# Kernel tuning notes

Measured on AMD Instinct MI355X. Metric: run time of the kernel, lower is better.

The kernel has to match this reference:

```python
import jax, jax.numpy as jnp
import numpy as np

N_LIG, N_PROT, K = 1024, 8192, 48
N = N_LIG + N_PROT
HID, FEAT, DEPTH = 256, 32, 5
NF = 6                      # sinusoid frequencies -> 12-dim distance embedding
EDGE_DIM = 4 * NF           # per-block dist emb (12) + top-level dist emb (12)
NORM = 5.0                  # agg_norm_factor
_FREQS = (2.0 * np.pi * 4.0 ** np.arange(NF) / 15.0).astype(np.float32)

def sin_emb(d2):
    # d2: [E,1] squared distances -> [E, 2*NF] sinusoidal embedding
    d = jnp.sqrt(d2 + 1e-8)
    x = d * _FREQS
    return jnp.concatenate([jnp.sin(x), jnp.cos(x)], axis=-1)

def knn_edges(coors):
    # KNN (k=48, no self loops) restricted to ligand query nodes (first N_LIG),
    # matching edges[:, :N_lig*k] slicing of knn_graph(flow='target_to_source').
    c = jax.lax.stop_gradient(coors)
    lig = c[:N_LIG]
    d2 = jnp.sum((lig[:, None, :] - c[None, :, :]) ** 2, axis=-1)  # [N_LIG, N]
    d2 = d2.at[jnp.arange(N_LIG), jnp.arange(N_LIG)].set(jnp.inf)
    _, idx = jax.lax.top_k(-d2, K)                                  # [N_LIG, K]
    row = jnp.repeat(jnp.arange(N_LIG), K)
    col = idx.reshape(-1)
    return row, col

def egnn(h, x, row, col, W_in, b_in, W_out, b_out, edge_W1, edge_b1, edge_W2, edge_b2, att_W, att_b, node_W1, node_b1, node_W2, node_b2, coord_W1, coord_b1, coord_W2, coord_b2, coord_W3):
    # EDM-style EGNN: per block 1 GCL (edge MLP + attention gate + node MLP residual)
    # followed by an equivariant coordinate update; sin distance embedding.
    emb0 = sin_emb(jnp.sum((x[row] - x[col]) ** 2, axis=-1, keepdims=True))
    h = h @ W_in + b_in
    for l in range(DEPTH):
        diff = x[row] - x[col]                         # [E,3]
        d2 = jnp.sum(diff ** 2, axis=-1, keepdims=True)
        cdiff = diff / (jnp.sqrt(d2 + 1e-8) + 1.0)     # norm_constant = 1
        ea = jnp.concatenate([sin_emb(d2), emb0], axis=-1)  # [E, EDGE_DIM]
        m = jax.nn.silu(jnp.concatenate([h[row], h[col], ea], axis=-1) @ edge_W1[l] + edge_b1[l])
        m = jax.nn.silu(m @ edge_W2[l] + edge_b2[l])
        m = m * jax.nn.sigmoid(m @ att_W[l] + att_b[l])         # attention gate
        agg = jax.ops.segment_sum(m, row, num_segments=N) / NORM
        u = jax.nn.silu(jnp.concatenate([h, agg], axis=-1) @ node_W1[l] + node_b1[l])
        h = h + (u @ node_W2[l] + node_b2[l])                    # residual node update
        c = jax.nn.silu(jnp.concatenate([h[row], h[col], ea], axis=-1) @ coord_W1[l] + coord_b1[l])  # use_latest_h
        c = jax.nn.silu(c @ coord_W2[l] + coord_b2[l])
        x = x + jax.ops.segment_sum(cdiff * (c @ coord_W3[l]), row, num_segments=N) / NORM
    return h @ W_out + b_out, x

def setup_inputs():
    key = jax.random.key(0)
    ks = jax.random.split(key, 24)
    f32 = jnp.float32
    def nrm(i, shape, scale=0.05):
        return jax.random.normal(ks[i], shape, dtype=f32) * scale
    return {
        'protein_positions': nrm(0, (N_PROT, 3), 3.0),
        'protein_ele': jax.random.randint(ks[1], (N_PROT,), 0, 5),
        'protein_amino_acid': jax.random.randint(ks[2], (N_PROT,), 0, 20),
        'protein_is_backbone': jax.random.randint(ks[3], (N_PROT,), 0, 2),
        'Xt_pos': nrm(4, (N_LIG, 3), 1.0),
        'Xt_features': nrm(5, (N_LIG, FEAT), 1.0),
        't': jax.random.randint(ks[6], (N_LIG,), 0, 1000),
        'Wt_time': nrm(7, (1000, 8), 1.0),
        'W_ele': nrm(8, (5, 16), 1.0),
        'W_aa': nrm(9, (20, 16), 1.0),
        'W_bb': nrm(10, (2, 8), 1.0),
        'W_in': nrm(11, (40, HID)), 'b_in': jnp.zeros((HID,), f32),
        'W_out': nrm(12, (HID, FEAT)), 'b_out': jnp.zeros((FEAT,), f32),
        'edge_W1': nrm(13, (DEPTH, 2 * HID + EDGE_DIM, HID)), 'edge_b1': jnp.zeros((DEPTH, HID), f32),
        'edge_W2': nrm(14, (DEPTH, HID, HID)), 'edge_b2': jnp.zeros((DEPTH, HID), f32),
        'att_W': nrm(15, (DEPTH, HID, 1)), 'att_b': jnp.zeros((DEPTH, 1), f32),
        'node_W1': nrm(16, (DEPTH, 2 * HID, HID)), 'node_b1': jnp.zeros((DEPTH, HID), f32),
        'node_W2': nrm(17, (DEPTH, HID, HID)), 'node_b2': jnp.zeros((DEPTH, HID), f32),
        'coord_W1': nrm(18, (DEPTH, 2 * HID + EDGE_DIM, HID)), 'coord_b1': jnp.zeros((DEPTH, HID), f32),
        'coord_W2': nrm(19, (DEPTH, HID, HID)), 'coord_b2': jnp.zeros((DEPTH, HID), f32),
        'coord_W3': nrm(20, (DEPTH, HID, 1), 0.001),
        'pos_w': jnp.ones((1, 1), f32),
    }

def reference(protein_positions, protein_ele, protein_amino_acid, protein_is_backbone, Xt_pos, Xt_features, t, Wt_time, W_ele, W_aa, W_bb, W_in, b_in, W_out, b_out, edge_W1, edge_b1, edge_W2, edge_b2, att_W, att_b, node_W1, node_b1, node_W2, node_b2, coord_W1, coord_b1, coord_W2, coord_b2, coord_W3, pos_w):
    prot_feat = jnp.concatenate([W_ele[protein_ele], W_aa[protein_amino_acid], W_bb[protein_is_backbone]], axis=-1)  # [N_PROT,40]
    feats = jnp.concatenate([jnp.concatenate([Xt_features, Wt_time[t]], axis=-1), prot_feat], axis=0)  # [N,40]
    coors = jnp.concatenate([Xt_pos, protein_positions], axis=0)  # [N,3]
    row, col = knn_edges(coors)
    h, x = egnn(feats, coors, row, col, W_in, b_in, W_out, b_out, edge_W1, edge_b1, edge_W2, edge_b2, att_W, att_b, node_W1, node_b1, node_W2, node_b2, coord_W1, coord_b1, coord_W2, coord_b2, coord_W3)
    # pos_linear: Linear(1,1,bias=False) applied elementwise == scalar multiply
    return x[:N_LIG] * pos_w[0, 0], h[:N_LIG]
```

## Files before the change

kernel.cpp:

```cpp
#include <hip/hip_runtime.h>
#include <hip/hip_bf16.h>
#include <math.h>

#define N_LIGC 1024
#define NTOT 9216
#define KNN 48
#define HID 256
#define DEPTHC 5
#define ETOT (N_LIGC*KNN)
#define KBINS 4096

typedef unsigned short u16;
typedef __attribute__((ext_vector_type(8))) short bf16x8;
typedef __attribute__((ext_vector_type(4))) float f32x4;

__device__ __forceinline__ float freq_f(int i){
  double p = (double)(1 << (2*i));
  return (float)((2.0*3.14159265358979323846)*p/15.0);
}
__device__ __forceinline__ float silu_f(float v){
  return v*__builtin_amdgcn_rcpf(1.0f+__expf(-v));
}
__device__ __forceinline__ float sigm_f(float v){
  return __builtin_amdgcn_rcpf(1.0f+__expf(-v));
}
// ... 19 lines not shown
  int Kt = Kp >> 5;
  int k0 = rest2 % Kt;
  int layer = rest2 / Kt;
  int kq = lane >> 4, nl = lane & 15;
  int kb = k0*32 + kq*8, n = n0*16 + nl;
  u16 o[8];
  #pragma unroll
  for (int j=0;j<8;j++){
    int k = kb + j;
    float v = (k < Keff) ? src[((size_t)layer*srcK + kOff + k)*N + n] : 0.f;
    o[j] = f2b_p(v);
  }
  *(uint4*)(dst + (size_t)idx*8) = *(uint4*)o;
}

__global__ __launch_bounds__(256) void k_packall(
    const float* eW1, const float* eW2, const float* nW1, const float* nW2,
    const float* cW1, const float* cW2, const float* Wout,
    u16* eW1abP, u16* eW1cP, u16* eW2p, u16* nW1p, u16* nW2p,
    u16* cW1abP, u16* cW1cP, u16* cW2p, u16* WoutP)
{
  int idx = blockIdx.x*256 + threadIdx.x;
  if (idx < 81920){ pack_one(eW1, eW1abP, 536, 0,   512, 512, 256, idx); return; } idx -= 81920;
  if (idx < 5120 ){ pack_one(eW1, eW1cP,  536, 512, 24,  32,  256, idx); return; } idx -= 5120;
  if (idx < 40960){ pack_one(eW2, eW2p,   256, 0,   256, 256, 256, idx); return; } idx -= 40960;
  if (idx < 81920){ pack_one(nW1, nW1p,   512, 0,   512, 512, 256, idx); return; } idx -= 81920;
  if (idx < 40960){ pack_one(nW2, nW2p,   256, 0,   256, 256, 256, idx); return; } idx -= 40960;
  if (idx < 81920){ pack_one(cW1, cW1abP, 536, 0,   512, 512, 256, idx); return; } idx -= 81920;
  if (idx < 5120 ){ pack_one(cW1, cW1cP,  536, 512, 24,  32,  256, idx); return; } idx -= 5120;
  if (idx < 40960){ pack_one(cW2, cW2p,   256, 0,   256, 256, 256, idx); return; } idx -= 40960;
  if (idx < 1024 ){ pack_one(Wout, WoutP, 256, 0,   256, 256, 32,  idx); return; }
}

__global__ __launch_bounds__(256) void k_embed_hinit(
    const float* __restrict__ protPos, const int* __restrict__ protEle,
    const int* __restrict__ protAA, const int* __restrict__ protBB,
    const float* __restrict__ XtPos, const float* __restrict__ XtFeat,
    const int* __restrict__ tArr, const float* __restrict__ WtTime,
    const float* __restrict__ Wele, const float* __restrict__ Waa,
    const float* __restrict__ Wbb,
    const float* __restrict__ Win, const float* __restrict__ bin,
    float* __restrict__ X0, float* __restrict__ X1,
    float* __restrict__ h, u16* __restrict__ h_bf)
{
  __shared__ float sF[8*40];
  int blk=blockIdx.x, tid=threadIdx.x;
  int n0=blk*8;
  for (int x=tid; x<344; x+=256){
    if (x < 320){
      int n = x/40, k = x%40;
      int node = n0+n;
      float v;
      if (node < N_LIGC){
        if (k < 32) v = XtFeat[node*32+k];
        else        v = WtTime[tArr[node]*8 + (k-32)];
      } else {
        int p = node - N_LIGC;
        if (k < 16)      v = Wele[protEle[p]*16 + k];
        else if (k < 32) v = Waa[protAA[p]*16 + (k-16)];
        else             v = Wbb[protBB[p]*8 + (k-32)];
      }
// ... 11 lines not shown
  #pragma unroll
  for (int n=0;n<8;n++) acc[n]=b;
  for (int k=0;k<40;k++){
    float w=Win[k*HID+tid];
    #pragma unroll
    for (int n=0;n<8;n++) acc[n]+=sF[n*40+k]*w;
  }
  #pragma unroll
  for (int n=0;n<8;n++){
    h[(size_t)(n0+n)*HID+tid]=acc[n];
    h_bf[(size_t)(n0+n)*HID+tid]=f2b_p(acc[n]);
  }
}

__global__ __launch_bounds__(256) void k_knn(const float* __restrict__ X,
    int* __restrict__ col, float* __restrict__ emb0)
{
  __shared__ unsigned int hist[KBINS];
  __shared__ unsigned int part[256];
  __shared__ float selD[KNN];
  __shared__ int   candI[512];
  __shared__ float candV[512];
  __shared__ int sB, sCless, sNeed, sNsel, sNcand;
  int b = blockIdx.x, tid = threadIdx.x;
  for (int i=tid;i<KBINS;i+=256) hist[i]=0u;
  if (tid==0){ sNsel=0; sNcand=0; }
  float px = X[b*3+0], py = X[b*3+1], pz = X[b*3+2];
  __syncthreads();
  #pragma unroll 4
  for (int j=0;j<36;j++){
    int i = tid + 256*j;
// ... 71 lines not shown
        int   os = __shfl_down(bslot, off);
        if (ov < bv || (ov==bv && oi<bi)){ bv=ov; bi=oi; bslot=os; }
      }
      int wslot = __shfl(bslot, 0);
      if (tid==0){ col[b*KNN+base+it]=bi; selD[base+it]=bv; }
      if ((wslot & 63) == tid) cv[wslot >> 6] = INFINITY;
    }
  }
  __syncthreads();
  if (tid < KNN){
    float d = sqrtf(selD[tid] + 1e-8f);
    int base = (b*KNN+tid)*12;
    #pragma unroll
    for (int i=0;i<6;i++){
      float fr = freq_f(i);
      emb0[base+i]   = sinf(d*fr);
      emb0[base+6+i] = cosf(d*fr);
    }
  }
}

__global__ __launch_bounds__(256) void k_pq(const u16* __restrict__ h_bf,
    const u16* __restrict__ Wab, float* __restrict__ R, u16* __restrict__ Qb, int l)
{
  __shared__ __align__(16) u16 sA[32*264];
  int blk=blockIdx.x, tid=threadIdx.x;
  int lane=tid&63, ng=tid>>6, quad=lane>>4, nl=lane&15;
  for (int t=tid; t<32*32; t+=256){
    int i=t>>5, q=t&31;
    uint4 v = ((const uint4*)(h_bf + (size_t)(blk*32+i)*HID))[q];
    *(uint4*)(sA + i*264 + q*8) = v;
  }
// ... 59 lines not shown
    #pragma unroll
    for (int nt=0;nt<4;nt++){
      int n = ng*64 + nt*16 + nl;
      #pragma unroll
      for (int r=0;r<4;r++){
        int node = blk*32 + mt*16 + quad*4 + r;
        R[(size_t)node*HID + n] = aR[mt][nt][r];
      }
    }
  }
}

__global__ __launch_bounds__(256,4) void k_comb_edge(
    const u16* __restrict__ Qb, const float* __restrict__ R,
    const float* __restrict__ xc,
    const int* __restrict__ colIdx, const float* __restrict__ emb0,
    const u16* __restrict__ W1cP, const float* __restrict__ B1,
    const u16* __restrict__ W2p, const float* __restrict__ B2,
    const float* __restrict__ attW, const float* __restrict__ attB,
    u16* __restrict__ agg_bf, int l)
{
  __shared__ __align__(16) u16 sQ[48*264];
  __shared__ __align__(16) u16 sEA[48*40];
  __shared__ float sR[256];
  __shared__ int sCol[48];
  __shared__ float sD[48];
  __shared__ float sSig[48];
  __shared__ float sDot[48][4];

  int row = blockIdx.x, tid = threadIdx.x;
  int lane = tid & 63, ng = tid >> 6;
// ... 2 lines not shown
  if (tid < 48) sCol[tid] = colIdx[(size_t)row*KNN + tid];
  sR[tid] = R[(size_t)row*HID + tid];
  __syncthreads();
  for (int t = tid; t < 48*32; t += 256){
    int e = t >> 5, q = t & 31;
    uint4 v = ((const uint4*)(Qb + (size_t)sCol[e]*HID))[q];
    *(uint4*)(sQ + e*264 + q*8) = v;
  }
  if (tid < 48){
    int cg = sCol[tid];
    float dx = xc[row*3+0]-xc[cg*3+0];
    float dy = xc[row*3+1]-xc[cg*3+1];
    float dz = xc[row*3+2]-xc[cg*3+2];
    float d = sqrtf(dx*dx+dy*dy+dz*dz + 1e-8f);
    sD[tid] = d;
    u16* ea = sEA + tid*40;
    #pragma unroll
    for (int i=0;i<12;i++) ea[12+i] = f2b_p(emb0[((size_t)row*KNN + tid)*12 + i]);
    #pragma unroll
    for (int i=24;i<32;i++) ea[i] = 0;
  }
  __syncthreads();
  for (int t=tid; t<288; t+=256){
    int e = t/6, i = t - 6*e;
    float fr = 0.41887903f * (float)(1 << (2*i));
    float x = sD[e]*fr;
    u16* ea = sEA + e*40;
    ea[i]   = f2b(__sinf(x));
    ea[6+i] = f2b(__cosf(x));
  }
  __syncthreads();

  f32x4 zero4 = {0.f,0.f,0.f,0.f};
// ... 113 lines not shown
    sgv[mt][r] = sSig[mt*16 + quad*4 + r];
  #pragma unroll
  for (int nt=0;nt<4;nt++){
    float a = 0.f;
    #pragma unroll
    for (int mt=0;mt<3;mt++)
    #pragma unroll
    for (int r=0;r<4;r++)
      a += acc2[mt][nt][r]*sgv[mt][r];
    a += __shfl_xor(a, 16);
    a += __shfl_xor(a, 32);
    if (quad == 0) agg_bf[(size_t)row*HID + ng*64 + nt*16 + nl] = f2b(a*0.2f);
  }
}

__global__ __launch_bounds__(256) void k_node(
    float* __restrict__ h, u16* __restrict__ h_bf,
    const u16* __restrict__ agg_bf,
    const u16* __restrict__ W1p, const float* __restrict__ B1,
    const u16* __restrict__ W2p, const float* __restrict__ B2,
    const u16* __restrict__ cWab, u16* __restrict__ QbC, float* __restrict__ RC,
    const u16* __restrict__ eWabN, u16* __restrict__ QbE, float* __restrict__ RE, int doE,
    const u16* __restrict__ WoutP, const float* __restrict__ bout,
    float* __restrict__ outH, int doOut, int l)
{
  __shared__ __align__(16) u16 sA[32*520];
  __shared__ __align__(16) u16 sU[32*264];
  u16* sH = sA;
  int blk=blockIdx.x, tid=threadIdx.x;
  int lane=tid&63, wv=tid>>6, quad=lane>>4, nl=lane&15;
  for (int t=tid; t<32*64; t+=256){
    int i=t>>6, q=t&63;
    int node = blk*32+i;
    uint4 v;
    if (q<32) v = ((const uint4*)(h_bf + (size_t)node*HID))[q];
    else if (node < N_LIGC) v = ((const uint4*)(agg_bf + (size_t)node*HID))[q-32];
    else { v.x=0u; v.y=0u; v.z=0u; v.w=0u; }
    *(uint4*)(sA + i*520 + q*8) = v;
  }
  __syncthreads();
  f32x4 zero4 = {0.f,0.f,0.f,0.f};
  f32x4 acc[2][4];
  #pragma unroll
  for (int i=0;i<2;i++){ acc[i][0]=zero4; acc[i][1]=zero4; acc[i][2]=zero4; acc[i][3]=zero4; }
  const u16* Wp = W1p + (size_t)l*512*HID;
  #pragma unroll 2
  for (int k0=0;k0<16;k0++){
    bf16x8 a0 = *(const bf16x8*)(sA + (0*16+nl)*520 + k0*32 + quad*8);
    bf16x8 a1 = *(const bf16x8*)(sA + (1*16+nl)*520 + k0*32 + quad*8);
    const u16* wb = Wp + ((size_t)(k0*16 + wv*4)*64 + lane)*8;
    bf16x8 b0 = *(const bf16x8*)(wb);
    bf16x8 b1 = *(const bf16x8*)(wb + 512);
    bf16x8 b2 = *(const bf16x8*)(wb + 1024);
    bf16x8 b3 = *(const bf16x8*)(wb + 1536);
    acc[0][0]=__builtin_amdgcn_mfma_f32_16x16x32_bf16(a0,b0,acc[0][0],0,0,0);
    acc[0][1]=__builtin_amdgcn_mfma_f32_16x16x32_bf16(a0,b1,acc[0][1],0,0,0);
    acc[0][2]=__builtin_amdgcn_mfma_f32_16x16x32_bf16(a0,b2,acc[0][2],0,0,0);
    acc[0][3]=__builtin_amdgcn_mfma_f32_16x16x32_bf16(a0,b3,acc[0][3],0,0,0);
    acc[1][0]=__builtin_amdgcn_mfma_f32_16x16x32_bf16(a1,b0,acc[1][0],0,0,0);
    acc[1][1]=__builtin_amdgcn_mfma_f32_16x16x32_bf16(a1,b1,acc[1][1],0,0,0);
    acc[1][2]=__builtin_amdgcn_mfma_f32_16x16x32_bf16(a1,b2,acc[1][2],0,0,0);
    acc[1][3]=__builtin_amdgcn_mfma_f32_16x16x32_bf16(a1,b3,acc[1][3],0,0,0);
  }
  #pragma unroll
  for (int mt=0;mt<2;mt++)
  #pragma unroll
  for (int nt=0;nt<4;nt++){
    int n = wv*64 + nt*16 + nl;
    float bb = B1[l*HID + n];
    #pragma unroll
    for (int r=0;r<4;r++){
      int m = mt*16 + quad*4 + r;
      sU[m*264 + n] = f2b(silu_f(acc[mt][nt][r] + bb));
    }
  }
  __syncthreads();
  f32x4 acc2[2][4];
  #pragma unroll
  for (int i=0;i<2;i++){ acc2[i][0]=zero4; acc2[i][1]=zero4; acc2[i][2]=zero4; acc2[i][3]=zero4; }
  const u16* W2 = W2p + (size_t)l*HID*HID;
  #pragma unroll 2
  for (int k0=0;k0<8;k0++){
    bf16x8 a0 = *(const bf16x8*)(sU + (0*16+nl)*264 + k0*32 + quad*8);
    bf16x8 a1 = *(const bf16x8*)(sU + (1*16+nl)*264 + k0*32 + quad*8);
    const u16* wb = W2 + ((size_t)(k0*16 + wv*4)*64 + lane)*8;
    bf16x8 b0 = *(const bf16x8*)(wb);
    bf16x8 b1 = *(const bf16x8*)(wb + 512);
    bf16x8 b2 = *(const bf16x8*)(wb + 1024);
    bf16x8 b3 = *(const bf16x8*)(wb + 1536);
    acc2[0][0]=__builtin_amdgcn_mfma_f32_16x16x32_bf16(a0,b0,acc2[0][0],0,0,0);
    acc2[0][1]=__builtin_amdgcn_mfma_f32_16x16x32_bf16(a0,b1,acc2[0][1],0,0,0);
    acc2[0][2]=__builtin_amdgcn_mfma_f32_16x16x32_bf16(a0,b2,acc2[0][2],0,0,0);
    acc2[0][3]=__builtin_amdgcn_mfma_f32_16x16x32_bf16(a0,b3,acc2[0][3],0,0,0);
    acc2[1][0]=__builtin_amdgcn_mfma_f32_16x16x32_bf16(a1,b0,acc2[1][0],0,0,0);
    acc2[1][1]=__builtin_amdgcn_mfma_f32_16x16x32_bf16(a1,b1,acc2[1][1],0,0,0);
    acc2[1][2]=__builtin_amdgcn_mfma_f32_16x16x32_bf16(a1,b2,acc2[1][2],0,0,0);
    acc2[1][3]=__builtin_amdgcn_mfma_f32_16x16x32_bf16(a1,b3,acc2[1][3],0,0,0);
  }
  #pragma unroll
  for (int mt=0;mt<2;mt++)
  #pragma unroll
  for (int nt=0;nt<4;nt++){
    int n = wv*64 + nt*16 + nl;
    float bb = B2[l*HID + n];
    #pragma unroll
    for (int r=0;r<4;r++){
      int m = mt*16 + quad*4 + r;
      size_t idx = (size_t)(blk*32+m)*HID + n;
      float v = h[idx] + acc2[mt][nt][r] + bb;
      h[idx] = v;
      u16 bv = f2b(v);
      h_bf[idx] = bv;
      sH[m*264 + n] = bv;
    }
  }
  __syncthreads();

  const u16* Wl = cWab + (size_t)l*512*HID;
  f32x4 q[2][4];
  #pragma unroll
  for (int i=0;i<2;i++){ q[i][0]=zero4; q[i][1]=zero4; q[i][2]=zero4; q[i][3]=zero4; }
  #pragma unroll 2
  for (int k0=0;k0<8;k0++){
    bf16x8 a0 = *(const bf16x8*)(sH + (0*16+nl)*264 + k0*32 + quad*8);
    bf16x8 a1 = *(const bf16x8*)(sH + (1*16+nl)*264 + k0*32 + quad*8);
    const u16* wb = Wl + ((size_t)((k0+8)*16 + wv*4)*64 + lane)*8;
    bf16x8 b0 = *(const bf16x8*)(wb);
    bf16x8 b1 = *(const bf16x8*)(wb + 512);
    bf16x8 b2 = *(const bf16x8*)(wb + 1024);
    bf16x8 b3 = *(const bf16x8*)(wb + 1536);
    q[0][0]=__builtin_amdgcn_mfma_f32_16x16x32_bf16(a0,b0,q[0][0],0,0,0);
    q[0][1]=__builtin_amdgcn_mfma_f32_16x16x32_bf16(a0,b1,q[0][1],0,0,0);
    q[0][2]=__builtin_amdgcn_mfma_f32_16x16x32_bf16(a0,b2,q[0][2],0,0,0);
    q[0][3]=__builtin_amdgcn_mfma_f32_16x16x32_bf16(a0,b3,q[0][3],0,0,0);
    q[1][0]=__builtin_amdgcn_mfma_f32_16x16x32_bf16(a1,b0,q[1][0],0,0,0);
    q[1][1]=__builtin_amdgcn_mfma_f32_16x16x32_bf16(a1,b1,q[1][1],0,0,0);
    q[1][2]=__builtin_amdgcn_mfma_f32_16x16x32_bf16(a1,b2,q[1][2],0,0,0);
    q[1][3]=__builtin_amdgcn_mfma_f32_16x16x32_bf16(a1,b3,q[1][3],0,0,0);
  }
  #pragma unroll
  for (int mt=0;mt<2;mt++)
  #pragma unroll
  for (int nt=0;nt<4;nt++){
    int n = wv*64 + nt*16 + nl;
    #pragma unroll
    for (int r=0;r<4;r++){
      int node = blk*32 + mt*16 + quad*4 + r;
      QbC[(size_t)node*HID + n] = f2b(q[mt][nt][r]);
    }
  }
  if (blk < 32){
    #pragma unroll
    for (int i=0;i<2;i++){ q[i][0]=zero4; q[i][1]=zero4; q[i][2]=zero4; q[i][3]=zero4; }
    #pragma unroll 2
    for (int k0=0;k0<8;k0++){
      bf16x8 a0 = *(const bf16x8*)(sH + (0*16+nl)*264 + k0*32 + quad*8);
      bf16x8 a1 = *(const bf16x8*)(sH + (1*16+nl)*264 + k0*32 + quad*8);
      const u16* wb = Wl + ((size_t)(k0*16 + wv*4)*64 + lane)*8;
      bf16x8 b0 = *(const bf16x8*)(wb);
      bf16x8 b1 = *(const bf16x8*)(wb + 512);
      bf16x8 b2 = *(const bf16x8*)(wb + 1024);
      bf16x8 b3 = *(const bf16x8*)(wb + 1536);
      q[0][0]=__builtin_amdgcn_mfma_f32_16x16x32_bf16(a0,b0,q[0][0],0,0,0);
      q[0][1]=__builtin_amdgcn_mfma_f32_16x16x32_bf16(a0,b1,q[0][1],0,0,0);
      q[0][2]=__builtin_amdgcn_mfma_f32_16x16x32_bf16(a0,b2,q[0][2],0,0,0);
      q[0][3]=__builtin_amdgcn_mfma_f32_16x16x32_bf16(a0,b3,q[0][3],0,0,0);
      q[1][0]=__builtin_amdgcn_mfma_f32_16x16x32_bf16(a1,b0,q[1][0],0,0,0);
      q[1][1]=__builtin_amdgcn_mfma_f32_16x16x32_bf16(a1,b1,q[1][1],0,0,0);
      q[1][2]=__builtin_amdgcn_mfma_f32_16x16x32_bf16(a1,b2,q[1][2],0,0,0);
      q[1][3]=__builtin_amdgcn_mfma_f32_16x16x32_bf16(a1,b3,q[1][3],0,0,0);
    }
    #pragma unroll
    for (int mt=0;mt<2;mt++)
    #pragma unroll
    for (int nt=0;nt<4;nt++){
      int n = wv*64 + nt*16 + nl;
      #pragma unroll
      for (int r=0;r<4;r++){
        int node = blk*32 + mt*16 + quad*4 + r;
        RC[(size_t)node*HID + n] = q[mt][nt][r];
      }
    }
  }
  if (doE){
    #pragma unroll
    for (int i=0;i<2;i++){ q[i][0]=zero4; q[i][1]=zero4; q[i][2]=zero4; q[i][3]=zero4; }
    #pragma unroll 2
    for (int k0=0;k0<8;k0++){
      bf16x8 a0 = *(const bf16x8*)(sH + (0*16+nl)*264 + k0*32 + quad*8);
      bf16x8 a1 = *(const bf16x8*)(sH + (1*16+nl)*264 + k0*32 + quad*8);
      const u16* wb = eWabN + ((size_t)((k0+8)*16 + wv*4)*64 + lane)*8;
      bf16x8 b0 = *(const bf16x8*)(wb);
      bf16x8 b1 = *(const bf16x8*)(wb + 512);
      bf16x8 b2 = *(const bf16x8*)(wb + 1024);
      bf16x8 b3 = *(const bf16x8*)(wb + 1536);
      q[0][0]=__builtin_amdgcn_mfma_f32_16x16x32_bf16(a0,b0,q[0][0],0,0,0);
      q[0][1]=__builtin_amdgcn_mfma_f32_16x16x32_bf16(a0,b1,q[0][1],0,0,0);
      q[0][2]=__builtin_amdgcn_mfma_f32_16x16x32_bf16(a0,b2,q[0][2],0,0,0);
      q[0][3]=__builtin_amdgcn_mfma_f32_16x16x32_bf16(a0,b3,q[0][3],0,0,0);
      q[1][0]=__builtin_amdgcn_mfma_f32_16x16x32_bf16(a1,b0,q[1][0],0,0,0);
      q[1][1]=__builtin_amdgcn_mfma_f32_16x16x32_bf16(a1,b1,q[1][1],0,0,0);
      q[1][2]=__builtin_amdgcn_mfma_f32_16x16x32_bf16(a1,b2,q[1][2],0,0,0);
      q[1][3]=__builtin_amdgcn_mfma_f32_16x16x32_bf16(a1,b3,q[1][3],0,0,0);
    }
    #pragma unroll
    for (int mt=0;mt<2;mt++)
    #pragma unroll
    for (int nt=0;nt<4;nt++){
      int n = wv*64 + nt*16 + nl;
      #pragma unroll
      for (int r=0;r<4;r++){
        int node = blk*32 + mt*16 + quad*4 + r;
        QbE[(size_t)node*HID + n] = f2b(q[mt][nt][r]);
      }
    }
    if (blk < 32){
      #pragma unroll
      for (int i=0;i<2;i++){ q[i][0]=zero4; q[i][1]=zero4; q[i][2]=zero4; q[i][3]=zero4; }
      #pragma unroll 2
      for (int k0=0;k0<8;k0++){
        bf16x8 a0 = *(const bf16x8*)(sH + (0*16+nl)*264 + k0*32 + quad*8);
        bf16x8 a1 = *(const bf16x8*)(sH + (1*16+nl)*264 + k0*32 + quad*8);
        const u16* wb = eWabN + ((size_t)(k0*16 + wv*4)*64 + lane)*8;
        bf16x8 b0 = *(const bf16x8*)(wb);
        bf16x8 b1 = *(const bf16x8*)(wb + 512);
        bf16x8 b2 = *(const bf16x8*)(wb + 1024);
        bf16x8 b3 = *(const bf16x8*)(wb + 1536);
        q[0][0]=__builtin_amdgcn_mfma_f32_16x16x32_bf16(a0,b0,q[0][0],0,0,0);
        q[0][1]=__builtin_amdgcn_mfma_f32_16x16x32_bf16(a0,b1,q[0][1],0,0,0);
        q[0][2]=__builtin_amdgcn_mfma_f32_16x16x32_bf16(a0,b2,q[0][2],0,0,0);
        q[0][3]=__builtin_amdgcn_mfma_f32_16x16x32_bf16(a0,b3,q[0][3],0,0,0);
        q[1][0]=__builtin_amdgcn_mfma_f32_16x16x32_bf16(a1,b0,q[1][0],0,0,0);
        q[1][1]=__builtin_amdgcn_mfma_f32_16x16x32_bf16(a1,b1,q[1][1],0,0,0);
        q[1][2]=__builtin_amdgcn_mfma_f32_16x16x32_bf16(a1,b2,q[1][2],0,0,0);
        q[1][3]=__builtin_amdgcn_mfma_f32_16x16x32_bf16(a1,b3,q[1][3],0,0,0);
      }
      #pragma unroll
      for (int mt=0;mt<2;mt++)
      #pragma unroll
      for (int nt=0;nt<4;nt++){
        int n = wv*64 + nt*16 + nl;
        #pragma unroll
        for (int r=0;r<4;r++){
          int node = blk*32 + mt*16 + quad*4 + r;
          RE[(size_t)node*HID + n] = q[mt][nt][r];
        }
      }
    }
  }
  if (doOut && blk < 32){
    int mt = wv >> 1, ntw = wv & 1;
    f32x4 o = zero4;
    #pragma unroll 2
    for (int k0=0;k0<8;k0++){
      bf16x8 a = *(const bf16x8*)(sH + (mt*16+nl)*264 + k0*32 + quad*8);
      bf16x8 b = *(const bf16x8*)(WoutP + ((size_t)(k0*2 + ntw)*64 + lane)*8);
      o = __builtin_amdgcn_mfma_f32_16x16x32_bf16(a,b,o,0,0,0);
    }
    int n = ntw*16 + nl;
    float bb = bout[n];
    #pragma unroll
    for (int r=0;r<4;r++){
      int m = mt*16 + quad*4 + r;
      outH[(size_t)(blk*32+m)*32 + n] = o[r] + bb;
    }
  }
}

__global__ __launch_bounds__(256,4) void k_comb_coord(
    const u16* __restrict__ Qb, const float* __restrict__ R,
    const float* __restrict__ xc, float* __restrict__ xn,
    const int* __restrict__ colIdx, const float* __restrict__ emb0,
    const u16* __restrict__ W1cP, const float* __restrict__ B1,
    const u16* __restrict__ W2p, const float* __restrict__ B2,
    const float* __restrict__ cW3,
    const float* __restrict__ posw, float* __restrict__ outX, int doOut, int l)
{
  __shared__ __align__(16) u16 sQ[48*264];
  __shared__ __align__(16) u16 sEA[48*40];
  __shared__ float sR[256];
  __shared__ int sCol[48];
  __shared__ float sD[48];
  __shared__ float sCd[48*3];
  __shared__ float sS[48];
  __shared__ float sDot[48][4];

  int row = blockIdx.x, tid = threadIdx.x;
// ... 5 lines not shown
  __syncthreads();
  for (int t = tid; t < 48*32; t += 256){
    int e = t >> 5, q = t & 31;
    uint4 v = ((const uint4*)(Qb + (size_t)sCol[e]*HID))[q];
    *(uint4*)(sQ + e*264 + q*8) = v;
  }
  if (tid < 48){
    int cg = sCol[tid];
    float dx = xc[row*3+0]-xc[cg*3+0];
    float dy = xc[row*3+1]-xc[cg*3+1];
    float dz = xc[row*3+2]-xc[cg*3+2];
    float d = sqrtf(dx*dx+dy*dy+dz*dz + 1e-8f);
    sD[tid] = d;
    float rden = __builtin_amdgcn_rcpf(d + 1.0f);
    sCd[tid*3+0]=dx*rden; sCd[tid*3+1]=dy*rden; sCd[tid*3+2]=dz*rden;
    u16* ea = sEA + tid*40;
    #pragma unroll
    for (int i=0;i<12;i++) ea[12+i] = f2b_p(emb0[((size_t)row*KNN + tid)*12 + i]);
    #pragma unroll
    for (int i=24;i<32;i++) ea[i] = 0;
  }
  __syncthreads();
  for (int t=tid; t<288; t+=256){
    int e = t/6, i = t - 6*e;
    float fr = 0.41887903f * (float)(1 << (2*i));
    float x = sD[e]*fr;
    u16* ea = sEA + e*40;
    ea[i]   = f2b(__sinf(x));
    ea[6+i] = f2b(__cosf(x));
  }
  __syncthreads();

  f32x4 zero4 = {0.f,0.f,0.f,0.f};
// ... 142 lines not shown
  const float* nW1     = (const float*)d_in[21];
  const float* nB1     = (const float*)d_in[22];
  const float* nW2     = (const float*)d_in[23];
  const float* nB2     = (const float*)d_in[24];
  const float* cW1     = (const float*)d_in[25];
  const float* cB1     = (const float*)d_in[26];
  const float* cW2     = (const float*)d_in[27];
  const float* cB2     = (const float*)d_in[28];
  const float* cW3     = (const float*)d_in[29];
  const float* posw    = (const float*)d_in[30];

  float* fp = (float*)d_ws;
  float* X0   = fp;               fp += NTOT*3;
  float* X1   = fp;               fp += NTOT*3;
  float* h    = fp;               fp += (size_t)NTOT*HID;
  float* emb0 = fp;               fp += (size_t)ETOT*12;
  float* RC   = fp;               fp += (size_t)N_LIGC*HID;
  float* RE   = fp;               fp += (size_t)N_LIGC*HID;
  int*   col  = (int*)fp;         fp += ETOT;
  u16*   up   = (u16*)fp;
  u16* h_bf   = up;               up += (size_t)NTOT*HID;
  u16* agg_bf = up;               up += (size_t)N_LIGC*HID;
  u16* QbE    = up;               up += (size_t)NTOT*HID;
  u16* QbC    = up;               up += (size_t)NTOT*HID;
  u16* eW1abP = up;               up += (size_t)DEPTHC*512*HID;
  u16* eW1cP  = up;               up += (size_t)DEPTHC*32*HID;
  u16* eW2p   = up;               up += (size_t)DEPTHC*HID*HID;
  u16* nW1p   = up;               up += (size_t)DEPTHC*512*HID;
  u16* nW2p   = up;               up += (size_t)DEPTHC*HID*HID;
  u16* cW1abP = up;               up += (size_t)DEPTHC*512*HID;
  u16* cW1cP  = up;               up += (size_t)DEPTHC*32*HID;
  u16* cW2p   = up;               up += (size_t)DEPTHC*HID*HID;
  u16* WoutP  = up;               up += (size_t)256*32;

  k_packall<<<1484,256,0,stream>>>(eW1,eW2,nW1,nW2,cW1,cW2,Wout,
      eW1abP,eW1cP,eW2p,nW1p,nW2p,cW1abP,cW1cP,cW2p,WoutP);
  k_embed_hinit<<<NTOT/8,256,0,stream>>>(protPos,protEle,protAA,protBB,XtPos,XtFeat,
      tArr,WtTime,Wele,Waa,Wbb,Win,bin,X0,X1,h,h_bf);
  k_knn<<<N_LIGC,256,0,stream>>>(X0,col,emb0);
  k_pq<<<NTOT/32,256,0,stream>>>(h_bf,eW1abP,RE,QbE,0);

  float* xc = X0; float* xn = X1;
  float* outF = (float*)d_out;
  for (int l=0;l<DEPTHC;l++){
    k_comb_edge<<<N_LIGC,256,0,stream>>>(QbE,RE,xc,col,emb0,eW1cP,eB1,eW2p,eB2,attW,attB,agg_bf,l);
    const u16* eNext = eW1abP + (size_t)((l+1)%DEPTHC)*512*HID;
    k_node<<<NTOT/32,256,0,stream>>>(h,h_bf,agg_bf,nW1p,nB1,nW2p,nB2,
        cW1abP,QbC,RC, eNext,QbE,RE,(l<DEPTHC-1)?1:0,
        WoutP,bout, outF+3072, (l==DEPTHC-1)?1:0, l);
    k_comb_coord<<<N_LIGC,256,0,stream>>>(QbC,RC,xc,xn,col,emb0,cW1cP,cB1,cW2p,cB2,cW3,
        posw, outF, (l==DEPTHC-1)?1:0, l);
    float* t2=xc; xc=xn; xn=t2;
  }
}
```

Baseline: 531.5 us.

## Halve node-kernel row tile, store emb0 as bf16, merge pack and embed kernels

The node kernel now processes 16 nodes per block instead of 32 (576 blocks) with smaller LDS and a 3-waves-per-SIMD occupancy hint. This raises parallelism but each block re-reads the full weight matrices, doubling weight traffic. The static distance embedding is stored as bf16 in the KNN kernel, so the edge and coord kernels copy it directly instead of converting per edge. The weight-packing and embedding/h-init kernels are fused into one launch to save a launch and let them overlap.

```diff
diff --git a/kernel.cpp b/kernel.cpp
--- a/kernel.cpp
+++ b/kernel.cpp
@@ -9,6 +9,7 @@
 #define DEPTHC 5
 #define ETOT (N_LIGC*KNN)
 #define KBINS 4096
+#define PACK_BLKS 1484
 
 typedef unsigned short u16;
 typedef __attribute__((ext_vector_type(8))) short bf16x8;
@@ -58,25 +59,11 @@
   *(uint4*)(dst + (size_t)idx*8) = *(uint4*)o;
 }
 
-__global__ __launch_bounds__(256) void k_packall(
+__global__ __launch_bounds__(256) void k_prep(
     const float* eW1, const float* eW2, const float* nW1, const float* nW2,
     const float* cW1, const float* cW2, const float* Wout,
     u16* eW1abP, u16* eW1cP, u16* eW2p, u16* nW1p, u16* nW2p,
-    u16* cW1abP, u16* cW1cP, u16* cW2p, u16* WoutP)
-{
-  int idx = blockIdx.x*256 + threadIdx.x;
-  if (idx < 81920){ pack_one(eW1, eW1abP, 536, 0,   512, 512, 256, idx); return; } idx -= 81920;
-  if (idx < 5120 ){ pack_one(eW1, eW1cP,  536, 512, 24,  32,  256, idx); return; } idx -= 5120;
-  if (idx < 40960){ pack_one(eW2, eW2p,   256, 0,   256, 256, 256, idx); return; } idx -= 40960;
-  if (idx < 81920){ pack_one(nW1, nW1p,   512, 0,   512, 512, 256, idx); return; } idx -= 81920;
-  if (idx < 40960){ pack_one(nW2, nW2p,   256, 0,   256, 256, 256, idx); return; } idx -= 40960;
-  if (idx < 81920){ pack_one(cW1, cW1abP, 536, 0,   512, 512, 256, idx); return; } idx -= 81920;
-  if (idx < 5120 ){ pack_one(cW1, cW1cP,  536, 512, 24,  32,  256, idx); return; } idx -= 5120;
-  if (idx < 40960){ pack_one(cW2, cW2p,   256, 0,   256, 256, 256, idx); return; } idx -= 40960;
-  if (idx < 1024 ){ pack_one(Wout, WoutP, 256, 0,   256, 256, 32,  idx); return; }
-}
-
-__global__ __launch_bounds__(256) void k_embed_hinit(
+    u16* cW1abP, u16* cW1cP, u16* cW2p, u16* WoutP,
     const float* __restrict__ protPos, const int* __restrict__ protEle,
     const int* __restrict__ protAA, const int* __restrict__ protBB,
     const float* __restrict__ XtPos, const float* __restrict__ XtFeat,
@@ -88,7 +75,20 @@
     float* __restrict__ h, u16* __restrict__ h_bf)
 {
   __shared__ float sF[8*40];
-  int blk=blockIdx.x, tid=threadIdx.x;
+  if (blockIdx.x < PACK_BLKS){
+    int idx = blockIdx.x*256 + threadIdx.x;
+    if (idx < 81920){ pack_one(eW1, eW1abP, 536, 0,   512, 512, 256, idx); return; } idx -= 81920;
+    if (idx < 5120 ){ pack_one(eW1, eW1cP,  536, 512, 24,  32,  256, idx); return; } idx -= 5120;
+    if (idx < 40960){ pack_one(eW2, eW2p,   256, 0,   256, 256, 256, idx); return; } idx -= 40960;
+    if (idx < 81920){ pack_one(nW1, nW1p,   512, 0,   512, 512, 256, idx); return; } idx -= 81920;
+    if (idx < 40960){ pack_one(nW2, nW2p,   256, 0,   256, 256, 256, idx); return; } idx -= 40960;
+    if (idx < 81920){ pack_one(cW1, cW1abP, 536, 0,   512, 512, 256, idx); return; } idx -= 81920;
+    if (idx < 5120 ){ pack_one(cW1, cW1cP,  536, 512, 24,  32,  256, idx); return; } idx -= 5120;
+    if (idx < 40960){ pack_one(cW2, cW2p,   256, 0,   256, 256, 256, idx); return; } idx -= 40960;
+    if (idx < 1024 ){ pack_one(Wout, WoutP, 256, 0,   256, 256, 32,  idx); return; }
+    return;
+  }
+  int blk=blockIdx.x - PACK_BLKS, tid=threadIdx.x;
   int n0=blk*8;
   for (int x=tid; x<344; x+=256){
     if (x < 320){
@@ -130,7 +130,7 @@
 }
 
 __global__ __launch_bounds__(256) void k_knn(const float* __restrict__ X,
-    int* __restrict__ col, float* __restrict__ emb0)
+    int* __restrict__ col, u16* __restrict__ emb0)
 {
   __shared__ unsigned int hist[KBINS];
   __shared__ unsigned int part[256];
@@ -232,8 +232,8 @@
     #pragma unroll
     for (int i=0;i<6;i++){
       float fr = freq_f(i);
-      emb0[base+i]   = sinf(d*fr);
-      emb0[base+6+i] = cosf(d*fr);
+      emb0[base+i]   = f2b_p(sinf(d*fr));
+      emb0[base+6+i] = f2b_p(cosf(d*fr));
     }
   }
 }
@@ -323,7 +323,7 @@
 __global__ __launch_bounds__(256,4) void k_comb_edge(
     const u16* __restrict__ Qb, const float* __restrict__ R,
     const float* __restrict__ xc,
-    const int* __restrict__ colIdx, const float* __restrict__ emb0,
+    const int* __restrict__ colIdx, const u16* __restrict__ emb0,
     const u16* __restrict__ W1cP, const float* __restrict__ B1,
     const u16* __restrict__ W2p, const float* __restrict__ B2,
     const float* __restrict__ attW, const float* __restrict__ attB,
@@ -356,9 +356,11 @@
     float dz = xc[row*3+2]-xc[cg*3+2];
     float d = sqrtf(dx*dx+dy*dy+dz*dz + 1e-8f);
     sD[tid] = d;
+    const unsigned int* ep = (const unsigned int*)(emb0 + ((size_t)row*KNN + tid)*12);
+    unsigned int* dd = (unsigned int*)(sEA + tid*40 + 12);
+    #pragma unroll
+    for (int i=0;i<6;i++) dd[i] = ep[i];
     u16* ea = sEA + tid*40;
-    #pragma unroll
-    for (int i=0;i<12;i++) ea[12+i] = f2b_p(emb0[((size_t)row*KNN + tid)*12 + i]);
     #pragma unroll
     for (int i=24;i<32;i++) ea[i] = 0;
   }
@@ -502,7 +504,7 @@
   }
 }
 
-__global__ __launch_bounds__(256) void k_node(
+__global__ __launch_bounds__(256,3) void k_node(
     float* __restrict__ h, u16* __restrict__ h_bf,
     const u16* __restrict__ agg_bf,
     const u16* __restrict__ W1p, const float* __restrict__ B1,
@@ -512,14 +514,14 @@
     const u16* __restrict__ WoutP, const float* __restrict__ bout,
     float* __restrict__ outH, int doOut, int l)
 {
-  __shared__ __align__(16) u16 sA[32*520];
-  __shared__ __align__(16) u16 sU[32*264];
+  __shared__ __align__(16) u16 sA[16*520];
+  __shared__ __align__(16) u16 sU[16*264];
   u16* sH = sA;
   int blk=blockIdx.x, tid=threadIdx.x;
   int lane=tid&63, wv=tid>>6, quad=lane>>4, nl=lane&15;
-  for (int t=tid; t<32*64; t+=256){
+  for (int t=tid; t<16*64; t+=256){
     int i=t>>6, q=t&63;
-    int node = blk*32+i;
+    int node = blk*16+i;
     uint4 v;
     if (q<32) v = ((const uint4*)(h_bf + (size_t)node*HID))[q];
     else if (node < N_LIGC) v = ((const uint4*)(agg_bf + (size_t)node*HID))[q-32];
@@ -528,74 +530,58 @@
   }
   __syncthreads();
   f32x4 zero4 = {0.f,0.f,0.f,0.f};
-  f32x4 acc[2][4];
-  #pragma unroll
-  for (int i=0;i<2;i++){ acc[i][0]=zero4; acc[i][1]=zero4; acc[i][2]=zero4; acc[i][3]=zero4; }
+  f32x4 acc[4];
+  acc[0]=zero4; acc[1]=zero4; acc[2]=zero4; acc[3]=zero4;
   const u16* Wp = W1p + (size_t)l*512*HID;
   #pragma unroll 2
   for (int k0=0;k0<16;k0++){
-    bf16x8 a0 = *(const bf16x8*)(sA + (0*16+nl)*520 + k0*32 + quad*8);
-    bf16x8 a1 = *(const bf16x8*)(sA + (1*16+nl)*520 + k0*32 + quad*8);
+    bf16x8 a0 = *(const bf16x8*)(sA + nl*520 + k0*32 + quad*8);
     const u16* wb = Wp + ((size_t)(k0*16 + wv*4)*64 + lane)*8;
     bf16x8 b0 = *(const bf16x8*)(wb);
     bf16x8 b1 = *(const bf16x8*)(wb + 512);
     bf16x8 b2 = *(const bf16x8*)(wb + 1024);
     bf16x8 b3 = *(const bf16x8*)(wb + 1536);
-    acc[0][0]=__builtin_amdgcn_mfma_f32_16x16x32_bf16(a0,b0,acc[0][0],0,0,0);
-    acc[0][1]=__builtin_amdgcn_mfma_f32_16x16x32_bf16(a0,b1,acc[0][1],0,0,0);
-    acc[0][2]=__builtin_amdgcn_mfma_f32_16x16x32_bf16(a0,b2,acc[0][2],0,0,0);
-    acc[0][3]=__builtin_amdgcn_mfma_f32_16x16x32_bf16(a0,b3,acc[0][3],0,0,0);
-    acc[1][0]=__builtin_amdgcn_mfma_f32_16x16x32_bf16(a1,b0,acc[1][0],0,0,0);
-    acc[1][1]=__builtin_amdgcn_mfma_f32_16x16x32_bf16(a1,b1,acc[1][1],0,0,0);
-    acc[1][2]=__builtin_amdgcn_mfma_f32_16x16x32_bf16(a1,b2,acc[1][2],0,0,0);
-    acc[1][3]=__builtin_amdgcn_mfma_f32_16x16x32_bf16(a1,b3,acc[1][3],0,0,0);
-  }
-  #pragma unroll
-  for (int mt=0;mt<2;mt++)
+    acc[0]=__builtin_amdgcn_mfma_f32_16x16x32_bf16(a0,b0,acc[0],0,0,0);
+    acc[1]=__builtin_amdgcn_mfma_f32_16x16x32_bf16(a0,b1,acc[1],0,0,0);
+    acc[2]=__builtin_amdgcn_mfma_f32_16x16x32_bf16(a0,b2,acc[2],0,0,0);
+    acc[3]=__builtin_amdgcn_mfma_f32_16x16x32_bf16(a0,b3,acc[3],0,0,0);
+  }
   #pragma unroll
   for (int nt=0;nt<4;nt++){
     int n = wv*64 + nt*16 + nl;
     float bb = B1[l*HID + n];
     #pragma unroll
     for (int r=0;r<4;r++){
-      int m = mt*16 + quad*4 + r;
-      sU[m*264 + n] = f2b(silu_f(acc[mt][nt][r] + bb));
-    }
-  }
-  __syncthreads();
-  f32x4 acc2[2][4];
-  #pragma unroll
-  for (int i=0;i<2;i++){ acc2[i][0]=zero4; acc2[i][1]=zero4; acc2[i][2]=zero4; acc2[i][3]=zero4; }
+      int m = quad*4 + r;
+      sU[m*264 + n] = f2b(silu_f(acc[nt][r] + bb));
+    }
+  }
+  __syncthreads();
+  f32x4 acc2[4];
+  acc2[0]=zero4; acc2[1]=zero4; acc2[2]=zero4; acc2[3]=zero4;
   const u16* W2 = W2p + (size_t)l*HID*HID;
   #pragma unroll 2
   for (int k0=0;k0<8;k0++){
-    bf16x8 a0 = *(const bf16x8*)(sU + (0*16+nl)*264 + k0*32 + quad*8);
-    bf16x8 a1 = *(const bf16x8*)(sU + (1*16+nl)*264 + k0*32 + quad*8);
+    bf16x8 a0 = *(const bf16x8*)(sU + nl*264 + k0*32 + quad*8);
     const u16* wb = W2 + ((size_t)(k0*16 + wv*4)*64 + lane)*8;
     bf16x8 b0 = *(const bf16x8*)(wb);
     bf16x8 b1 = *(const bf16x8*)(wb + 512);
     bf16x8 b2 = *(const bf16x8*)(wb + 1024);
     bf16x8 b3 = *(const bf16x8*)(wb + 1536);
-    acc2[0][0]=__builtin_amdgcn_mfma_f32_16x16x32_bf16(a0,b0,acc2[0][0],0,0,0);
-    acc2[0][1]=__builtin_amdgcn_mfma_f32_16x16x32_bf16(a0,b1,acc2[0][1],0,0,0);
-    acc2[0][2]=__builtin_amdgcn_mfma_f32_16x16x32_bf16(a0,b2,acc2[0][2],0,0,0);
-    acc2[0][3]=__builtin_amdgcn_mfma_f32_16x16x32_bf16(a0,b3,acc2[0][3],0,0,0);
-    acc2[1][0]=__builtin_amdgcn_mfma_f32_16x16x32_bf16(a1,b0,acc2[1][0],0,0,0);
-    acc2[1][1]=__builtin_amdgcn_mfma_f32_16x16x32_bf16(a1,b1,acc2[1][1],0,0,0);
-    acc2[1][2]=__builtin_amdgcn_mfma_f32_16x16x32_bf16(a1,b2,acc2[1][2],0,0,0);
-    acc2[1][3]=__builtin_amdgcn_mfma_f32_16x16x32_bf16(a1,b3,acc2[1][3],0,0,0);
-  }
-  #pragma unroll
-  for (int mt=0;mt<2;mt++)
+    acc2[0]=__builtin_amdgcn_mfma_f32_16x16x32_bf16(a0,b0,acc2[0],0,0,0);
+    acc2[1]=__builtin_amdgcn_mfma_f32_16x16x32_bf16(a0,b1,acc2[1],0,0,0);
+    acc2[2]=__builtin_amdgcn_mfma_f32_16x16x32_bf16(a0,b2,acc2[2],0,0,0);
+    acc2[3]=__builtin_amdgcn_mfma_f32_16x16x32_bf16(a0,b3,acc2[3],0,0,0);
+  }
   #pragma unroll
   for (int nt=0;nt<4;nt++){
     int n = wv*64 + nt*16 + nl;
     float bb = B2[l*HID + n];
     #pragma unroll
     for (int r=0;r<4;r++){
-      int m = mt*16 + quad*4 + r;
-      size_t idx = (size_t)(blk*32+m)*HID + n;
-      float v = h[idx] + acc2[mt][nt][r] + bb;
+      int m = quad*4 + r;
+      size_t idx = (size_t)(blk*16+m)*HID + n;
+      float v = h[idx] + acc2[nt][r] + bb;
       h[idx] = v;
       u16 bv = f2b(v);
       h_bf[idx] = bv;
@@ -605,143 +591,111 @@
   __syncthreads();
 
   const u16* Wl = cWab + (size_t)l*512*HID;
-  f32x4 q[2][4];
-  #pragma unroll
-  for (int i=0;i<2;i++){ q[i][0]=zero4; q[i][1]=zero4; q[i][2]=zero4; q[i][3]=zero4; }
+  f32x4 q[4];
+  q[0]=zero4; q[1]=zero4; q[2]=zero4; q[3]=zero4;
   #pragma unroll 2
   for (int k0=0;k0<8;k0++){
-    bf16x8 a0 = *(const bf16x8*)(sH + (0*16+nl)*264 + k0*32 + quad*8);
-    bf16x8 a1 = *(const bf16x8*)(sH + (1*16+nl)*264 + k0*32 + quad*8);
+    bf16x8 a0 = *(const bf16x8*)(sH + nl*264 + k0*32 + quad*8);
     const u16* wb = Wl + ((size_t)((k0+8)*16 + wv*4)*64 + lane)*8;
     bf16x8 b0 = *(const bf16x8*)(wb);
     bf16x8 b1 = *(const bf16x8*)(wb + 512);
     bf16x8 b2 = *(const bf16x8*)(wb + 1024);
     bf16x8 b3 = *(const bf16x8*)(wb + 1536);
-    q[0][0]=__builtin_amdgcn_mfma_f32_16x16x32_bf16(a0,b0,q[0][0],0,0,0);
-    q[0][1]=__builtin_amdgcn_mfma_f32_16x16x32_bf16(a0,b1,q[0][1],0,0,0);
-    q[0][2]=__builtin_amdgcn_mfma_f32_16x16x32_bf16(a0,b2,q[0][2],0,0,0);
-    q[0][3]=__builtin_amdgcn_mfma_f32_16x16x32_bf16(a0,b3,q[0][3],0,0,0);
-    q[1][0]=__builtin_amdgcn_mfma_f32_16x16x32_bf16(a1,b0,q[1][0],0,0,0);
-    q[1][1]=__builtin_amdgcn_mfma_f32_16x16x32_bf16(a1,b1,q[1][1],0,0,0);
-    q[1][2]=__builtin_amdgcn_mfma_f32_16x16x32_bf16(a1,b2,q[1][2],0,0,0);
-    q[1][3]=__builtin_amdgcn_mfma_f32_16x16x32_bf16(a1,b3,q[1][3],0,0,0);
-  }
-  #pragma unroll
-  for (int mt=0;mt<2;mt++)
+    q[0]=__builtin_amdgcn_mfma_f32_16x16x32_bf16(a0,b0,q[0],0,0,0);
+    q[1]=__builtin_amdgcn_mfma_f32_16x16x32_bf16(a0,b1,q[1],0,0,0);
+    q[2]=__builtin_amdgcn_mfma_f32_16x16x32_bf16(a0,b2,q[2],0,0,0);
+    q[3]=__builtin_amdgcn_mfma_f32_16x16x32_bf16(a0,b3,q[3],0,0,0);
+  }
   #pragma unroll
   for (int nt=0;nt<4;nt++){
     int n = wv*64 + nt*16 + nl;
     #pragma unroll
     for (int r=0;r<4;r++){
-      int node = blk*32 + mt*16 + quad*4 + r;
-      QbC[(size_t)node*HID + n] = f2b(q[mt][nt][r]);
-    }
-  }
-  if (blk < 32){
-    #pragma unroll
-    for (int i=0;i<2;i++){ q[i][0]=zero4; q[i][1]=zero4; q[i][2]=zero4; q[i][3]=zero4; }
+      int node = blk*16 + quad*4 + r;
+      QbC[(size_t)node*HID + n] = f2b(q[nt][r]);
+    }
+  }
+  if (blk < 64){
+    q[0]=zero4; q[1]=zero4; q[2]=zero4; q[3]=zero4;
     #pragma unroll 2
     for (int k0=0;k0<8;k0++){
-      bf16x8 a0 = *(const bf16x8*)(sH + (0*16+nl)*264 + k0*32 + quad*8);
-      bf16x8 a1 = *(const bf16x8*)(sH + (1*16+nl)*264 + k0*32 + quad*8);
+      bf16x8 a0 = *(const bf16x8*)(sH + nl*264 + k0*32 + quad*8);
       const u16* wb = Wl + ((size_t)(k0*16 + wv*4)*64 + lane)*8;
       bf16x8 b0 = *(const bf16x8*)(wb);
       bf16x8 b1 = *(const bf16x8*)(wb + 512);
       bf16x8 b2 = *(const bf16x8*)(wb + 1024);
       bf16x8 b3 = *(const bf16x8*)(wb + 1536);
-      q[0][0]=__builtin_amdgcn_mfma_f32_16x16x32_bf16(a0,b0,q[0][0],0,0,0);
-      q[0][1]=__builtin_amdgcn_mfma_f32_16x16x32_bf16(a0,b1,q[0][1],0,0,0);
-      q[0][2]=__builtin_amdgcn_mfma_f32_16x16x32_bf16(a0,b2,q[0][2],0,0,0);
-      q[0][3]=__builtin_amdgcn_mfma_f32_16x16x32_bf16(a0,b3,q[0][3],0,0,0);
-      q[1][0]=__builtin_amdgcn_mfma_f32_16x16x32_bf16(a1,b0,q[1][0],0,0,0);
-      q[1][1]=__builtin_amdgcn_mfma_f32_16x16x32_bf16(a1,b1,q[1][1],0,0,0);
-      q[1][2]=__builtin_amdgcn_mfma_f32_16x16x32_bf16(a1,b2,q[1][2],0,0,0);
-      q[1][3]=__builtin_amdgcn_mfma_f32_16x16x32_bf16(a1,b3,q[1][3],0,0,0);
-    }
-    #pragma unroll
-    for (int mt=0;mt<2;mt++)
+      q[0]=__builtin_amdgcn_mfma_f32_16x16x32_bf16(a0,b0,q[0],0,0,0);
+      q[1]=__builtin_amdgcn_mfma_f32_16x16x32_bf16(a0,b1,q[1],0,0,0);
+      q[2]=__builtin_amdgcn_mfma_f32_16x16x32_bf16(a0,b2,q[2],0,0,0);
+      q[3]=__builtin_amdgcn_mfma_f32_16x16x32_bf16(a0,b3,q[3],0,0,0);
+    }
     #pragma unroll
     for (int nt=0;nt<4;nt++){
       int n = wv*64 + nt*16 + nl;
       #pragma unroll
       for (int r=0;r<4;r++){
-        int node = blk*32 + mt*16 + quad*4 + r;
-        RC[(size_t)node*HID + n] = q[mt][nt][r];
+        int node = blk*16 + quad*4 + r;
+        RC[(size_t)node*HID + n] = q[nt][r];
       }
     }
   }
   if (doE){
-    #pragma unroll
-    for (int i=0;i<2;i++){ q[i][0]=zero4; q[i][1]=zero4; q[i][2]=zero4; q[i][3]=zero4; }
+    q[0]=zero4; q[1]=zero4; q[2]=zero4; q[3]=zero4;
     #pragma unroll 2
     for (int k0=0;k0<8;k0++){
-      bf16x8 a0 = *(const bf16x8*)(sH + (0*16+nl)*264 + k0*32 + quad*8);
-      bf16x8 a1 = *(const bf16x8*)(sH + (1*16+nl)*264 + k0*32 + quad*8);
+      bf16x8 a0 = *(const bf16x8*)(sH + nl*264 + k0*32 + quad*8);
       const u16* wb = eWabN + ((size_t)((k0+8)*16 + wv*4)*64 + lane)*8;
       bf16x8 b0 = *(const bf16x8*)(wb);
       bf16x8 b1 = *(const bf16x8*)(wb + 512);
       bf16x8 b2 = *(const bf16x8*)(wb + 1024);
       bf16x8 b3 = *(const bf16x8*)(wb + 1536);
-      q[0][0]=__builtin_amdgcn_mfma_f32_16x16x32_bf16(a0,b0,q[0][0],0,0,0);
-      q[0][1]=__builtin_amdgcn_mfma_f32_16x16x32_bf16(a0,b1,q[0][1],0,0,0);
-      q[0][2]=__builtin_amdgcn_mfma_f32_16x16x32_bf16(a0,b2,q[0][2],0,0,0);
-      q[0][3]=__builtin_amdgcn_mfma_f32_16x16x32_bf16(a0,b3,q[0][3],0,0,0);
-      q[1][0]=__builtin_amdgcn_mfma_f32_16x16x32_bf16(a1,b0,q[1][0],0,0,0);
-      q[1][1]=__builtin_amdgcn_mfma_f32_16x16x32_bf16(a1,b1,q[1][1],0,0,0);
-      q[1][2]=__builtin_amdgcn_mfma_f32_16x16x32_bf16(a1,b2,q[1][2],0,0,0);
-      q[1][3]=__builtin_amdgcn_mfma_f32_16x16x32_bf16(a1,b3,q[1][3],0,0,0);
-    }
-    #pragma unroll
-    for (int mt=0;mt<2;mt++)
+      q[0]=__builtin_amdgcn_mfma_f32_16x16x32_bf16(a0,b0,q[0],0,0,0);
+      q[1]=__builtin_amdgcn_mfma_f32_16x16x32_bf16(a0,b1,q[1],0,0,0);
+      q[2]=__builtin_amdgcn_mfma_f32_16x16x32_bf16(a0,b2,q[2],0,0,0);
+      q[3]=__builtin_amdgcn_mfma_f32_16x16x32_bf16(a0,b3,q[3],0,0,0);
+    }
     #pragma unroll
     for (int nt=0;nt<4;nt++){
       int n = wv*64 + nt*16 + nl;
       #pragma unroll
       for (int r=0;r<4;r++){
-        int node = blk*32 + mt*16 + quad*4 + r;
-        QbE[(size_t)node*HID + n] = f2b(q[mt][nt][r]);
+        int node = blk*16 + quad*4 + r;
+        QbE[(size_t)node*HID + n] = f2b(q[nt][r]);
       }
     }
-    if (blk < 32){
-      #pragma unroll
-      for (int i=0;i<2;i++){ q[i][0]=zero4; q[i][1]=zero4; q[i][2]=zero4; q[i][3]=zero4; }
+    if (blk < 64){
+      q[0]=zero4; q[1]=zero4; q[2]=zero4; q[3]=zero4;
       #pragma unroll 2
       for (int k0=0;k0<8;k0++){
-        bf16x8 a0 = *(const bf16x8*)(sH + (0*16+nl)*264 + k0*32 + quad*8);
-        bf16x8 a1 = *(const bf16x8*)(sH + (1*16+nl)*264 + k0*32 + quad*8);
+        bf16x8 a0 = *(const bf16x8*)(sH + nl*264 + k0*32 + quad*8);
         const u16* wb = eWabN + ((size_t)(k0*16 + wv*4)*64 + lane)*8;
         bf16x8 b0 = *(const bf16x8*)(wb);
         bf16x8 b1 = *(const bf16x8*)(wb + 512);
         bf16x8 b2 = *(const bf16x8*)(wb + 1024);
         bf16x8 b3 = *(const bf16x8*)(wb + 1536);
-        q[0][0]=__builtin_amdgcn_mfma_f32_16x16x32_bf16(a0,b0,q[0][0],0,0,0);
-        q[0][1]=__builtin_amdgcn_mfma_f32_16x16x32_bf16(a0,b1,q[0][1],0,0,0);
-        q[0][2]=__builtin_amdgcn_mfma_f32_16x16x32_bf16(a0,b2,q[0][2],0,0,0);
-        q[0][3]=__builtin_amdgcn_mfma_f32_16x16x32_bf16(a0,b3,q[0][3],0,0,0);
-        q[1][0]=__builtin_amdgcn_mfma_f32_16x16x32_bf16(a1,b0,q[1][0],0,0,0);
-        q[1][1]=__builtin_amdgcn_mfma_f32_16x16x32_bf16(a1,b1,q[1][1],0,0,0);
-        q[1][2]=__builtin_amdgcn_mfma_f32_16x16x32_bf16(a1,b2,q[1][2],0,0,0);
-        q[1][3]=__builtin_amdgcn_mfma_f32_16x16x32_bf16(a1,b3,q[1][3],0,0,0);
+        q[0]=__builtin_amdgcn_mfma_f32_16x16x32_bf16(a0,b0,q[0],0,0,0);
+        q[1]=__builtin_amdgcn_mfma_f32_16x16x32_bf16(a0,b1,q[1],0,0,0);
+        q[2]=__builtin_amdgcn_mfma_f32_16x16x32_bf16(a0,b2,q[2],0,0,0);
+        q[3]=__builtin_amdgcn_mfma_f32_16x16x32_bf16(a0,b3,q[3],0,0,0);
       }
-      #pragma unroll
-      for (int mt=0;mt<2;mt++)
       #pragma unroll
       for (int nt=0;nt<4;nt++){
         int n = wv*64 + nt*16 + nl;
         #pragma unroll
         for (int r=0;r<4;r++){
-          int node = blk*32 + mt*16 + quad*4 + r;
-          RE[(size_t)node*HID + n] = q[mt][nt][r];
+          int node = blk*16 + quad*4 + r;
+          RE[(size_t)node*HID + n] = q[nt][r];
         }
       }
     }
   }
-  if (doOut && blk < 32){
-    int mt = wv >> 1, ntw = wv & 1;
+  if (doOut && blk < 64 && wv < 2){
+    int ntw = wv;
     f32x4 o = zero4;
     #pragma unroll 2
     for (int k0=0;k0<8;k0++){
-      bf16x8 a = *(const bf16x8*)(sH + (mt*16+nl)*264 + k0*32 + quad*8);
+      bf16x8 a = *(const bf16x8*)(sH + nl*264 + k0*32 + quad*8);
       bf16x8 b = *(const bf16x8*)(WoutP + ((size_t)(k0*2 + ntw)*64 + lane)*8);
       o = __builtin_amdgcn_mfma_f32_16x16x32_bf16(a,b,o,0,0,0);
     }
@@ -749,8 +703,8 @@
     float bb = bout[n];
     #pragma unroll
     for (int r=0;r<4;r++){
-      int m = mt*16 + quad*4 + r;
-      outH[(size_t)(blk*32+m)*32 + n] = o[r] + bb;
+      int m = quad*4 + r;
+      outH[(size_t)(blk*16+m)*32 + n] = o[r] + bb;
     }
   }
 }
@@ -758,7 +712,7 @@
 __global__ __launch_bounds__(256,4) void k_comb_coord(
     const u16* __restrict__ Qb, const float* __restrict__ R,
     const float* __restrict__ xc, float* __restrict__ xn,
-    const int* __restrict__ colIdx, const float* __restrict__ emb0,
+    const int* __restrict__ colIdx, const u16* __restrict__ emb0,
     const u16* __restrict__ W1cP, const float* __restrict__ B1,
     const u16* __restrict__ W2p, const float* __restrict__ B2,
     const float* __restrict__ cW3,
@@ -794,9 +748,11 @@
     sD[tid] = d;
     float rden = __builtin_amdgcn_rcpf(d + 1.0f);
     sCd[tid*3+0]=dx*rden; sCd[tid*3+1]=dy*rden; sCd[tid*3+2]=dz*rden;
+    const unsigned int* ep = (const unsigned int*)(emb0 + ((size_t)row*KNN + tid)*12);
+    unsigned int* dd = (unsigned int*)(sEA + tid*40 + 12);
+    #pragma unroll
+    for (int i=0;i<6;i++) dd[i] = ep[i];
     u16* ea = sEA + tid*40;
-    #pragma unroll
-    for (int i=0;i<12;i++) ea[12+i] = f2b_p(emb0[((size_t)row*KNN + tid)*12 + i]);
     #pragma unroll
     for (int i=24;i<32;i++) ea[i] = 0;
   }
@@ -969,11 +925,11 @@
   float* X0   = fp;               fp += NTOT*3;
   float* X1   = fp;               fp += NTOT*3;
   float* h    = fp;               fp += (size_t)NTOT*HID;
-  float* emb0 = fp;               fp += (size_t)ETOT*12;
   float* RC   = fp;               fp += (size_t)N_LIGC*HID;
   float* RE   = fp;               fp += (size_t)N_LIGC*HID;
   int*   col  = (int*)fp;         fp += ETOT;
   u16*   up   = (u16*)fp;
+  u16* emb0   = up;               up += (size_t)ETOT*12;
   u16* h_bf   = up;               up += (size_t)NTOT*HID;
   u16* agg_bf = up;               up += (size_t)N_LIGC*HID;
   u16* QbE    = up;               up += (size_t)NTOT*HID;
@@ -988,9 +944,9 @@
   u16* cW2p   = up;               up += (size_t)DEPTHC*HID*HID;
   u16* WoutP  = up;               up += (size_t)256*32;
 
-  k_packall<<<1484,256,0,stream>>>(eW1,eW2,nW1,nW2,cW1,cW2,Wout,
-      eW1abP,eW1cP,eW2p,nW1p,nW2p,cW1abP,cW1cP,cW2p,WoutP);
-  k_embed_hinit<<<NTOT/8,256,0,stream>>>(protPos,protEle,protAA,protBB,XtPos,XtFeat,
+  k_prep<<<PACK_BLKS + NTOT/8,256,0,stream>>>(eW1,eW2,nW1,nW2,cW1,cW2,Wout,
+      eW1abP,eW1cP,eW2p,nW1p,nW2p,cW1abP,cW1cP,cW2p,WoutP,
+      protPos,protEle,protAA,protBB,XtPos,XtFeat,
       tArr,WtTime,Wele,Waa,Wbb,Win,bin,X0,X1,h,h_bf);
   k_knn<<<N_LIGC,256,0,stream>>>(X0,col,emb0);
   k_pq<<<NTOT/32,256,0,stream>>>(h_bf,eW1abP,RE,QbE,0);
@@ -1000,7 +956,7 @@
   for (int l=0;l<DEPTHC;l++){
     k_comb_edge<<<N_LIGC,256,0,stream>>>(QbE,RE,xc,col,emb0,eW1cP,eB1,eW2p,eB2,attW,attB,agg_bf,l);
     const u16* eNext = eW1abP + (size_t)((l+1)%DEPTHC)*512*HID;
-    k_node<<<NTOT/32,256,0,stream>>>(h,h_bf,agg_bf,nW1p,nB1,nW2p,nB2,
+    k_node<<<NTOT/16,256,0,stream>>>(h,h_bf,agg_bf,nW1p,nB1,nW2p,nB2,
         cW1abP,QbC,RC, eNext,QbE,RE,(l<DEPTHC-1)?1:0,
         WoutP,bout, outF+3072, (l==DEPTHC-1)?1:0, l);
     k_comb_coord<<<N_LIGC,256,0,stream>>>(QbC,RC,xc,xn,col,emb0,cW1cP,cB1,cW2p,cB2,cW3,
```

Measured after the change: 540.7 us. About the same (+1.7%).
